# Performance work log

Hardware: AMD Instinct MI355X
Metric: run time of the kernel (lower is better)

## Reference

```python
import jax, jax.numpy as jnp
import numpy as np

BATCH, SEQ_LEN, D_MODEL, STATE_N, N_CLASSES = 32, 4096, 256, 64, 5


def setup_inputs() -> dict:
    key = jax.random.key(0)
    ks = jax.random.split(key, 9)
    x = jax.random.normal(ks[0], (BATCH, SEQ_LEN), jnp.float32)
    w_in = jax.random.normal(ks[1], (D_MODEL,), jnp.float32)
    b_in = jax.random.normal(ks[2], (D_MODEL,), jnp.float32) * 0.1
    # stable diagonal transition in (0.9, 0.999)
    A_diag = 0.9 + 0.099 * jax.random.uniform(ks[3], (D_MODEL, STATE_N), jnp.float32)
    B_in = jax.random.normal(ks[4], (D_MODEL, STATE_N), jnp.float32) * 0.1
    C_out = jax.random.normal(ks[5], (D_MODEL, STATE_N), jnp.float32) * 0.1
    D_skip = jax.random.normal(ks[6], (D_MODEL,), jnp.float32)
    W_head = jax.random.normal(ks[7], (2 * D_MODEL, N_CLASSES), jnp.float32) * 0.05
    b_head = jnp.zeros((N_CLASSES,), jnp.float32)
    return {"x": x, "w_in": w_in, "b_in": b_in, "A_diag": A_diag, "B_in": B_in,
            "C_out": C_out, "D_skip": D_skip, "W_head": W_head, "b_head": b_head}


def reference(x, w_in, b_in, A_diag, B_in, C_out, D_skip, W_head, b_head):
    # x: [B, T] scalar ECG signal; diagonal SSM recurrence over T via lax.scan
    Bsz = x.shape[0]
    D, N = A_diag.shape

    def step(s, xt):
        # xt: [B] scalar input at time t; project to channels
        u = xt[:, None] * w_in + b_in              # [B, D]
        s = A_diag * s + B_in * u[:, :, None]      # [B, D, N]
        h = jax.nn.gelu(jnp.einsum('bdn,dn->bd', s, C_out) + D_skip * u)  # [B, D]
        return s, h

    s0 = jnp.zeros((Bsz, D, N), x.dtype)
    _, h_all = jax.lax.scan(step, s0, x.T)         # h_all: [T, B, D]
    avg_p = h_all.mean(axis=0)                     # [B, D]
    max_p = h_all.max(axis=0)                      # [B, D]
    pooled = jnp.concatenate([avg_p, max_p], axis=-1)  # [B, 2D] (streaming_pool='avgmax')
    return pooled @ W_head + b_head                # [B, n_classes]
```

## Files before the change

### kernel.cpp

```cpp
#include <hip/hip_runtime.h>

#define BATCH 32
#define SEQ 4096
#define DMODEL 256
#define NCLS 5

typedef short          s8v __attribute__((ext_vector_type(8)));
typedef unsigned short u8v __attribute__((ext_vector_type(8)));
typedef float          f4v __attribute__((ext_vector_type(4)));

__device__ __forceinline__ unsigned short f2b(float f) {
    unsigned u = __float_as_uint(f);
    u += 0x7FFFu + ((u >> 16) & 1u);
    return (unsigned short)(u >> 16);
}
__device__ __forceinline__ float b2f(unsigned short u) {
    return __uint_as_float(((unsigned)u) << 16);
}

__global__ __launch_bounds__(512) void ssm_mfma_kernel(
    const float* __restrict__ x,
    const float* __restrict__ w_in,
    const float* __restrict__ b_in,
    const float* __restrict__ A_diag,
    const float* __restrict__ B_in,
    const float* __restrict__ C_out,
    const float* __restrict__ D_skip,
    float* __restrict__ pooled)
{
    __shared__ unsigned short MAb [64 * 72];
    __shared__ unsigned short CATb[64 * 72];
    __shared__ unsigned short TGb [64 * 72];
    __shared__ unsigned short Xb  [128 * 72];
    __shared__ unsigned short Sigb[128 * 72];
    __shared__ float XAf[128 * 65];
    __shared__ float Pf[64], Qf[64], Gf[64], Hf[64], Hcp[64];
    __shared__ float ps[8 * 32], pm[8 * 32];

    const int tid  = threadIdx.x;
    const int lane = tid & 63;
    const int wid  = tid >> 6;
    const int m16  = lane & 15;
    const int q4   = (lane >> 4) * 4;
    const int q8   = (lane >> 4) * 8;
    const int cb   = wid * 16;
    const int d    = blockIdx.x;

    const int   n  = lane;
    const float An = A_diag[d * 64 + n];
    const float CB = B_in[d * 64 + n] * C_out[d * 64 + n];
    const float wd = w_in[d], bd = b_in[d];
    const float Pn = CB * wd;
    const float Qn = CB * bd;
    const float Dw = D_skip[d] * wd;
    const float Db = D_skip[d] * bd;

    if (tid < 64) {
        Pf[n] = Pn; Qf[n] = Qn;
        float p = 1.0f;
        for (int m = 0; m <= 64; ++m) { XAf[m * 64 + n] = p; p *= An; }
    }
    __syncthreads();
    const float A64 = XAf[64 * 64 + n];
    const float cQ  = Qn * (1.0f - A64) / (1.0f - An);

    {
        const int r0 = tid >> 3, c0 = (tid & 7) * 8;
        #pragma unroll
        for (int jj = 0; jj < 8; ++jj) {
            const int j = c0 + jj;
            MAb [r0 * 72 + j] = f2b(XAf[(63 - j) * 64 + r0]);
            CATb[r0 * 72 + j] = f2b(XAf[(r0 + 1) * 64 + j]);
        }
        if (tid < 64) {
            float g = 0.0f, h = 0.0f;
            for (int nn = 0; nn < 64; ++nn) {
                const float pw = XAf[tid * 64 + nn];
                g = fmaf(pw, Pf[nn], g);
                h = fmaf(pw, Qf[nn], h);
            }
            Gf[tid] = g; Hf[tid] = h;
        }
    }
    __syncthreads();
    {
        const int k0 = tid >> 3, c0 = (tid & 7) * 8;
        #pragma unroll
        for (int jj = 0; jj < 8; ++jj) {
            const int j = c0 + jj;
            TGb[k0 * 72 + j] = (j <= k0) ? f2b(Gf[k0 - j]) : (unsigned short)0;
        }
        if (tid < 64) {
            float a = Db;
            for (int m = 0; m <= tid; ++m) a += Hf[m];
            Hcp[tid] = a;
        }
    }
    __syncthreads();

    s8v aMA[4][2], aCAT[4][2], aTG[4][2];
    #pragma unroll
    for (int rt = 0; rt < 4; ++rt)
        #pragma unroll
        for (int kb = 0; kb < 2; ++kb) {
            const int off = (rt * 16 + m16) * 72 + kb * 32 + q8;
            aMA [rt][kb] = *(const s8v*)&MAb [off];
            aCAT[rt][kb] = *(const s8v*)&CATb[off];
            aTG [rt][kb] = *(const s8v*)&TGb [off];
        }

    const int colA = tid >> 2;
    const int j0A  = (tid & 3) * 16;
    const float* xrow = x + (colA & 31) * SEQ + (colA >> 5) * 64 + j0A;
    unsigned short* xdst = &Xb[colA * 72 + j0A];

    float sig[4] = {0.0f, 0.0f, 0.0f, 0.0f};
    float psum = 0.0f, pmax = -1e30f;

    for (int g = 0; g < 16; ++g) {
        const float4* xg = (const float4*)(xrow + g * 256);
        const float4 u0 = xg[0], u1 = xg[1], u2 = xg[2], u3 = xg[3];
        u8v lo, hi;
        lo[0]=f2b(u0.x); lo[1]=f2b(u0.y); lo[2]=f2b(u0.z); lo[3]=f2b(u0.w);
        lo[4]=f2b(u1.x); lo[5]=f2b(u1.y); lo[6]=f2b(u1.z); lo[7]=f2b(u1.w);
        hi[0]=f2b(u2.x); hi[1]=f2b(u2.y); hi[2]=f2b(u2.z); hi[3]=f2b(u2.w);
        hi[4]=f2b(u3.x); hi[5]=f2b(u3.y); hi[6]=f2b(u3.z); hi[7]=f2b(u3.w);
        *(u8v*)(xdst)     = lo;
        *(u8v*)(xdst + 8) = hi;
        __syncthreads();

        const s8v bx0 = *(const s8v*)&Xb[(cb + m16) * 72 + q8];
        const s8v bx1 = *(const s8v*)&Xb[(cb + m16) * 72 + 32 + q8];
        #pragma unroll
        for (int rt = 0; rt < 4; ++rt) {
            f4v acc = {0.0f, 0.0f, 0.0f, 0.0f};
            acc = __builtin_amdgcn_mfma_f32_16x16x32_bf16(aMA[rt][0], bx0, acc, 0, 0, 0);
            acc = __builtin_amdgcn_mfma_f32_16x16x32_bf16(aMA[rt][1], bx1, acc, 0, 0, 0);
            #pragma unroll
            for (int r = 0; r < 4; ++r)
                XAf[(cb + m16) * 65 + rt * 16 + q4 + r] = acc[r];
        }
        __syncthreads();

        #pragma unroll
        for (int c = 0; c < 4; ++c) {
            #pragma unroll
            for (int i = 0; i < 4; ++i) {
                const int col = c * 32 + wid * 4 + i;
                Sigb[col * 72 + n] = f2b(sig[i]);
                sig[i] = fmaf(A64, sig[i], fmaf(Pn, XAf[col * 65 + n], cQ));
            }
        }
        __syncthreads();

        const s8v bs0 = *(const s8v*)&Sigb[(cb + m16) * 72 + q8];
        const s8v bs1 = *(const s8v*)&Sigb[(cb + m16) * 72 + 32 + q8];
        #pragma unroll
        for (int rt = 0; rt < 4; ++rt) {
            f4v acc = {0.0f, 0.0f, 0.0f, 0.0f};
            acc = __builtin_amdgcn_mfma_f32_16x16x32_bf16(aCAT[rt][0], bs0, acc, 0, 0, 0);
            acc = __builtin_amdgcn_mfma_f32_16x16x32_bf16(aCAT[rt][1], bs1, acc, 0, 0, 0);
            acc = __builtin_amdgcn_mfma_f32_16x16x32_bf16(aTG [rt][0], bx0, acc, 0, 0, 0);
            acc = __builtin_amdgcn_mfma_f32_16x16x32_bf16(aTG [rt][1], bx1, acc, 0, 0, 0);
            #pragma unroll
            for (int r = 0; r < 4; ++r) {
                const int k  = rt * 16 + q4 + r;
                const float xv = b2f(Xb[(cb + m16) * 72 + k]);
                const float yt = acc[r] + Hcp[k] + Dw * xv;
                const float y2 = yt * yt;
                const float zn = yt * fmaf(-0.07135481627f, y2, -1.5957691216f);
                const float h  = yt * __builtin_amdgcn_rcpf(1.0f + __expf(zn));
                psum += h;
                pmax = fmaxf(pmax, h);
            }
        }
        __syncthreads();
    }

    psum += __shfl_xor(psum, 16, 64); psum += __shfl_xor(psum, 32, 64);
    pmax = fmaxf(pmax, __shfl_xor(pmax, 16, 64));
    pmax = fmaxf(pmax, __shfl_xor(pmax, 32, 64));
    if (lane < 16) {
        ps[wid * 32 + (wid & 1) * 16 + lane] = psum;
        pm[wid * 32 + (wid & 1) * 16 + lane] = pmax;
    } else if (lane < 32) {
        const int ob = (((wid & 1) ^ 1) * 16) + (lane & 15);
        ps[wid * 32 + ob] = 0.0f;
        pm[wid * 32 + ob] = -1e30f;
    }
    __syncthreads();
    if (tid < 32) {
        float s = 0.0f, m = -1e30f;
        #pragma unroll
        for (int w = 0; w < 8; ++w) {
            s += ps[w * 32 + tid];
            m = fmaxf(m, pm[w * 32 + tid]);
        }
        pooled[tid * (2 * DMODEL) + d]          = s * (1.0f / SEQ);
        pooled[tid * (2 * DMODEL) + DMODEL + d] = m;
    }
}

__global__ __launch_bounds__(64) void head_kernel(
    const float* __restrict__ pooled,
    const float* __restrict__ W_head,
    const float* __restrict__ b_head,
    float* __restrict__ out)
{
    const int b = blockIdx.x, l = threadIdx.x;
    const float* p = pooled + b * (2 * DMODEL);
    float acc[NCLS] = {0, 0, 0, 0, 0};
    for (int k = l; k < 2 * DMODEL; k += 64) {
        const float pv = p[k];
        #pragma unroll
        for (int c = 0; c < NCLS; ++c)
            acc[c] = fmaf(pv, W_head[k * NCLS + c], acc[c]);
    }
    #pragma unroll
    for (int off = 32; off; off >>= 1)
        #pragma unroll
        for (int c = 0; c < NCLS; ++c) acc[c] += __shfl_xor(acc[c], off, 64);
    if (l == 0)
        #pragma unroll
        for (int c = 0; c < NCLS; ++c) out[b * NCLS + c] = acc[c] + b_head[c];
}

extern "C" void kernel_launch(void* const* d_in, const int* in_sizes, int n_in,
                              void* d_out, int out_size, void* d_ws, size_t ws_size,
                              hipStream_t stream) {
    const float* x      = (const float*)d_in[0];
    const float* w_in   = (const float*)d_in[1];
    const float* b_in   = (const float*)d_in[2];
    const float* A_diag = (const float*)d_in[3];
    const float* B_in   = (const float*)d_in[4];
    const float* C_out  = (const float*)d_in[5];
    const float* D_skip = (const float*)d_in[6];
    const float* W_head = (const float*)d_in[7];
    const float* b_head = (const float*)d_in[8];
    float* pooled = (float*)d_ws;
    float* out    = (float*)d_out;

    ssm_mfma_kernel<<<DMODEL, 512, 0, stream>>>(x, w_in, b_in, A_diag, B_in,
                                                C_out, D_skip, pooled);
    head_kernel<<<BATCH, 64, 0, stream>>>(pooled, W_head, b_head, out);
}
```

Measured before the change: 118.0 us.

## Remap batch columns per wave and replace chunk-state scan with in-register DPP scan

Each wave now owns four batch sequences laid out so the cross-chunk state recurrence can be done in registers with DPP row shifts and a ds_swizzle, instead of writing MFMA results to a float LDS buffer and scanning them serially with block-wide barriers. All __syncthreads in the time loop are removed, the next x chunk is prefetched from global while the current one is processed, and the bias terms (cQ, Hcp, the Dw skip) are folded into the MFMA accumulator initialisers and the Toeplitz matrix. Setup reductions are parallelised with shuffles, and the final pooling reduces within each wave. The intra-wave cross-lane data flow is intricate and depends on exact lane mappings, so a mistake would give wrong results rather than a slowdown.

```diff
diff --git a/kernel.cpp b/kernel.cpp
--- a/kernel.cpp
+++ b/kernel.cpp
@@ -5,17 +5,27 @@
 #define DMODEL 256
 #define NCLS 5
 
-typedef short          s8v __attribute__((ext_vector_type(8)));
-typedef unsigned short u8v __attribute__((ext_vector_type(8)));
-typedef float          f4v __attribute__((ext_vector_type(4)));
+typedef short          s8v  __attribute__((ext_vector_type(8)));
+typedef unsigned short u8v  __attribute__((ext_vector_type(8)));
+typedef unsigned short u4v  __attribute__((ext_vector_type(4)));
+typedef float          f4v  __attribute__((ext_vector_type(4)));
 
 __device__ __forceinline__ unsigned short f2b(float f) {
     unsigned u = __float_as_uint(f);
     u += 0x7FFFu + ((u >> 16) & 1u);
     return (unsigned short)(u >> 16);
 }
-__device__ __forceinline__ float b2f(unsigned short u) {
-    return __uint_as_float(((unsigned)u) << 16);
+__device__ __forceinline__ float dpp_shr4(float v) {
+    return __int_as_float(__builtin_amdgcn_update_dpp(
+        0, __float_as_int(v), 0x114, 0xF, 0xF, true));
+}
+__device__ __forceinline__ float dpp_shr8(float v) {
+    return __int_as_float(__builtin_amdgcn_update_dpp(
+        0, __float_as_int(v), 0x118, 0xF, 0xF, true));
+}
+__device__ __forceinline__ float swz_or12(float v) {
+    return __int_as_float(__builtin_amdgcn_ds_swizzle(
+        __float_as_int(v), 0x019F));
 }
 
 __global__ __launch_bounds__(512) void ssm_mfma_kernel(
@@ -28,72 +38,80 @@
     const float* __restrict__ D_skip,
     float* __restrict__ pooled)
 {
+    __shared__ float          Pow [65 * 64];
     __shared__ unsigned short MAb [64 * 72];
     __shared__ unsigned short CATb[64 * 72];
     __shared__ unsigned short TGb [64 * 72];
     __shared__ unsigned short Xb  [128 * 72];
     __shared__ unsigned short Sigb[128 * 72];
-    __shared__ float XAf[128 * 65];
-    __shared__ float Pf[64], Qf[64], Gf[64], Hf[64], Hcp[64];
-    __shared__ float ps[8 * 32], pm[8 * 32];
+    __shared__ float Pf[64], Qf[64], Gf[64], Hf[64], HcpS[64], Anf[64];
 
     const int tid  = threadIdx.x;
     const int lane = tid & 63;
     const int wid  = tid >> 6;
     const int m16  = lane & 15;
-    const int q4   = (lane >> 4) * 4;
-    const int q8   = (lane >> 4) * 8;
-    const int cb   = wid * 16;
+    const int q    = lane >> 4;
+    const int q4   = q * 4;
+    const int q8   = q * 8;
     const int d    = blockIdx.x;
 
-    const int   n  = lane;
-    const float An = A_diag[d * 64 + n];
-    const float CB = B_in[d * 64 + n] * C_out[d * 64 + n];
     const float wd = w_in[d], bd = b_in[d];
-    const float Pn = CB * wd;
-    const float Qn = CB * bd;
     const float Dw = D_skip[d] * wd;
     const float Db = D_skip[d] * bd;
 
+    const int bcol = wid * 4 + (m16 & 3);
+    const int cch  = m16 >> 2;
+    const int pcol = wid * 16 + m16;
+    const float* xrow = x + bcol * SEQ + cch * 64 + q * 16;
+    unsigned short* xdst = &Xb[pcol * 72 + q * 16];
+
+    float4 xl0 = ((const float4*)xrow)[0];
+    float4 xl1 = ((const float4*)xrow)[1];
+    float4 xl2 = ((const float4*)xrow)[2];
+    float4 xl3 = ((const float4*)xrow)[3];
+
     if (tid < 64) {
-        Pf[n] = Pn; Qf[n] = Qn;
+        const int n = tid;
+        const float An = A_diag[d * 64 + n];
+        const float CB = B_in[d * 64 + n] * C_out[d * 64 + n];
+        Anf[n] = An; Pf[n] = CB * wd; Qf[n] = CB * bd;
         float p = 1.0f;
-        for (int m = 0; m <= 64; ++m) { XAf[m * 64 + n] = p; p *= An; }
+        for (int m = 0; m <= 64; ++m) { Pow[m * 64 + n] = p; p *= An; }
     }
     __syncthreads();
-    const float A64 = XAf[64 * 64 + n];
-    const float cQ  = Qn * (1.0f - A64) / (1.0f - An);
-
+    {
+        const int mrow = tid >> 3, p8 = (tid & 7) * 8;
+        float g = 0.0f, h = 0.0f;
+        #pragma unroll
+        for (int jj = 0; jj < 8; ++jj) {
+            const float pw = Pow[mrow * 64 + p8 + jj];
+            g = fmaf(pw, Pf[p8 + jj], g);
+            h = fmaf(pw, Qf[p8 + jj], h);
+        }
+        g += __shfl_xor(g, 1, 64); g += __shfl_xor(g, 2, 64); g += __shfl_xor(g, 4, 64);
+        h += __shfl_xor(h, 1, 64); h += __shfl_xor(h, 2, 64); h += __shfl_xor(h, 4, 64);
+        if ((tid & 7) == 0) { Gf[mrow] = g; Hf[mrow] = h; }
+    }
+    __syncthreads();
     {
         const int r0 = tid >> 3, c0 = (tid & 7) * 8;
         #pragma unroll
         for (int jj = 0; jj < 8; ++jj) {
             const int j = c0 + jj;
-            MAb [r0 * 72 + j] = f2b(XAf[(63 - j) * 64 + r0]);
-            CATb[r0 * 72 + j] = f2b(XAf[(r0 + 1) * 64 + j]);
+            MAb [r0 * 72 + j] = f2b(Pf[r0] * Pow[(63 - j) * 64 + r0]);
+            CATb[r0 * 72 + j] = f2b(Pow[(r0 + 1) * 64 + j]);
+            TGb [r0 * 72 + j] = (j < r0)  ? f2b(Gf[r0 - j])
+                              : (j == r0) ? f2b(Gf[0] + Dw)
+                                          : (unsigned short)0;
         }
         if (tid < 64) {
-            float g = 0.0f, h = 0.0f;
-            for (int nn = 0; nn < 64; ++nn) {
-                const float pw = XAf[tid * 64 + nn];
-                g = fmaf(pw, Pf[nn], g);
-                h = fmaf(pw, Qf[nn], h);
+            float v = Hf[tid];
+            #pragma unroll
+            for (int dl = 1; dl < 64; dl <<= 1) {
+                const float t = __shfl(v, (tid - dl) & 63, 64);
+                v += (tid >= dl) ? t : 0.0f;
             }
-            Gf[tid] = g; Hf[tid] = h;
-        }
-    }
-    __syncthreads();
-    {
-        const int k0 = tid >> 3, c0 = (tid & 7) * 8;
-        #pragma unroll
-        for (int jj = 0; jj < 8; ++jj) {
-            const int j = c0 + jj;
-            TGb[k0 * 72 + j] = (j <= k0) ? f2b(Gf[k0 - j]) : (unsigned short)0;
-        }
-        if (tid < 64) {
-            float a = Db;
-            for (int m = 0; m <= tid; ++m) a += Hf[m];
-            Hcp[tid] = a;
+            HcpS[tid] = v + Db;
         }
     }
     __syncthreads();
@@ -108,65 +126,90 @@
             aCAT[rt][kb] = *(const s8v*)&CATb[off];
             aTG [rt][kb] = *(const s8v*)&TGb [off];
         }
-
-    const int colA = tid >> 2;
-    const int j0A  = (tid & 3) * 16;
-    const float* xrow = x + (colA & 31) * SEQ + (colA >> 5) * 64 + j0A;
-    unsigned short* xdst = &Xb[colA * 72 + j0A];
-
-    float sig[4] = {0.0f, 0.0f, 0.0f, 0.0f};
+    f4v cq[4], hcp[4];
+    float a64v[4][4], sig0[4][4];
+    #pragma unroll
+    for (int rt = 0; rt < 4; ++rt)
+        #pragma unroll
+        for (int r = 0; r < 4; ++r) {
+            const int nn = rt * 16 + q4 + r;
+            const float A64 = Pow[64 * 64 + nn];
+            a64v[rt][r] = A64;
+            cq[rt][r]   = Qf[nn] * (1.0f - A64) / (1.0f - Anf[nn]);
+            hcp[rt][r]  = HcpS[nn];
+            sig0[rt][r] = 0.0f;
+        }
+    const bool cc1 = (cch & 1) != 0;
+    const bool cc2 = (cch & 2) != 0;
+
+    {
+        u8v lo, hi;
+        lo[0]=f2b(xl0.x); lo[1]=f2b(xl0.y); lo[2]=f2b(xl0.z); lo[3]=f2b(xl0.w);
+        lo[4]=f2b(xl1.x); lo[5]=f2b(xl1.y); lo[6]=f2b(xl1.z); lo[7]=f2b(xl1.w);
+        hi[0]=f2b(xl2.x); hi[1]=f2b(xl2.y); hi[2]=f2b(xl2.z); hi[3]=f2b(xl2.w);
+        hi[4]=f2b(xl3.x); hi[5]=f2b(xl3.y); hi[6]=f2b(xl3.z); hi[7]=f2b(xl3.w);
+        *(u8v*)xdst       = lo;
+        *(u8v*)(xdst + 8) = hi;
+    }
+
     float psum = 0.0f, pmax = -1e30f;
 
+    #pragma unroll 1
     for (int g = 0; g < 16; ++g) {
-        const float4* xg = (const float4*)(xrow + g * 256);
-        const float4 u0 = xg[0], u1 = xg[1], u2 = xg[2], u3 = xg[3];
-        u8v lo, hi;
-        lo[0]=f2b(u0.x); lo[1]=f2b(u0.y); lo[2]=f2b(u0.z); lo[3]=f2b(u0.w);
-        lo[4]=f2b(u1.x); lo[5]=f2b(u1.y); lo[6]=f2b(u1.z); lo[7]=f2b(u1.w);
-        hi[0]=f2b(u2.x); hi[1]=f2b(u2.y); hi[2]=f2b(u2.z); hi[3]=f2b(u2.w);
-        hi[4]=f2b(u3.x); hi[5]=f2b(u3.y); hi[6]=f2b(u3.z); hi[7]=f2b(u3.w);
-        *(u8v*)(xdst)     = lo;
-        *(u8v*)(xdst + 8) = hi;
-        __syncthreads();
-
-        const s8v bx0 = *(const s8v*)&Xb[(cb + m16) * 72 + q8];
-        const s8v bx1 = *(const s8v*)&Xb[(cb + m16) * 72 + 32 + q8];
+        float4 yl0, yl1, yl2, yl3;
+        if (g < 15) {
+            const float4* xg = (const float4*)(xrow + (g + 1) * 256);
+            yl0 = xg[0]; yl1 = xg[1]; yl2 = xg[2]; yl3 = xg[3];
+        }
+        const s8v bx0 = *(const s8v*)&Xb[pcol * 72 + q8];
+        const s8v bx1 = *(const s8v*)&Xb[pcol * 72 + 32 + q8];
+        f4v vB[4];
         #pragma unroll
         for (int rt = 0; rt < 4; ++rt) {
-            f4v acc = {0.0f, 0.0f, 0.0f, 0.0f};
-            acc = __builtin_amdgcn_mfma_f32_16x16x32_bf16(aMA[rt][0], bx0, acc, 0, 0, 0);
-            acc = __builtin_amdgcn_mfma_f32_16x16x32_bf16(aMA[rt][1], bx1, acc, 0, 0, 0);
+            vB[rt] = __builtin_amdgcn_mfma_f32_16x16x32_bf16(aMA[rt][0], bx0, cq[rt], 0, 0, 0);
+            vB[rt] = __builtin_amdgcn_mfma_f32_16x16x32_bf16(aMA[rt][1], bx1, vB[rt], 0, 0, 0);
+        }
+        if (g < 15) {
+            u8v lo, hi;
+            lo[0]=f2b(yl0.x); lo[1]=f2b(yl0.y); lo[2]=f2b(yl0.z); lo[3]=f2b(yl0.w);
+            lo[4]=f2b(yl1.x); lo[5]=f2b(yl1.y); lo[6]=f2b(yl1.z); lo[7]=f2b(yl1.w);
+            hi[0]=f2b(yl2.x); hi[1]=f2b(yl2.y); hi[2]=f2b(yl2.z); hi[3]=f2b(yl2.w);
+            hi[4]=f2b(yl3.x); hi[5]=f2b(yl3.y); hi[6]=f2b(yl3.z); hi[7]=f2b(yl3.w);
+            *(u8v*)xdst       = lo;
+            *(u8v*)(xdst + 8) = hi;
+        }
+        #pragma unroll
+        for (int rt = 0; rt < 4; ++rt) {
+            u4v sg;
             #pragma unroll
-            for (int r = 0; r < 4; ++r)
-                XAf[(cb + m16) * 65 + rt * 16 + q4 + r] = acc[r];
-        }
-        __syncthreads();
-
-        #pragma unroll
-        for (int c = 0; c < 4; ++c) {
-            #pragma unroll
-            for (int i = 0; i < 4; ++i) {
-                const int col = c * 32 + wid * 4 + i;
-                Sigb[col * 72 + n] = f2b(sig[i]);
-                sig[i] = fmaf(A64, sig[i], fmaf(Pn, XAf[col * 65 + n], cQ));
+            for (int r = 0; r < 4; ++r) {
+                const float a  = a64v[rt][r];
+                const float a2 = a * a;
+                const float v  = vB[rt][r];
+                const float t1 = dpp_shr4(v);
+                const float i1 = fmaf(a, t1, v);
+                const float t2 = dpp_shr8(i1);
+                const float e  = fmaf(a, t2, t1);
+                const float ac = (cc1 ? a : 1.0f) * (cc2 ? a2 : 1.0f);
+                const float se = fmaf(ac, sig0[rt][r], e);
+                const float i2 = fmaf(a, e, v);
+                const float S  = swz_or12(i2);
+                sig0[rt][r] = fmaf(a2 * a2, sig0[rt][r], S);
+                sg[r] = f2b(se);
             }
-        }
-        __syncthreads();
-
-        const s8v bs0 = *(const s8v*)&Sigb[(cb + m16) * 72 + q8];
-        const s8v bs1 = *(const s8v*)&Sigb[(cb + m16) * 72 + 32 + q8];
+            *(u4v*)&Sigb[pcol * 72 + rt * 16 + q4] = sg;
+        }
+        const s8v bs0 = *(const s8v*)&Sigb[pcol * 72 + q8];
+        const s8v bs1 = *(const s8v*)&Sigb[pcol * 72 + 32 + q8];
         #pragma unroll
         for (int rt = 0; rt < 4; ++rt) {
-            f4v acc = {0.0f, 0.0f, 0.0f, 0.0f};
-            acc = __builtin_amdgcn_mfma_f32_16x16x32_bf16(aCAT[rt][0], bs0, acc, 0, 0, 0);
+            f4v acc = __builtin_amdgcn_mfma_f32_16x16x32_bf16(aCAT[rt][0], bs0, hcp[rt], 0, 0, 0);
             acc = __builtin_amdgcn_mfma_f32_16x16x32_bf16(aCAT[rt][1], bs1, acc, 0, 0, 0);
             acc = __builtin_amdgcn_mfma_f32_16x16x32_bf16(aTG [rt][0], bx0, acc, 0, 0, 0);
             acc = __builtin_amdgcn_mfma_f32_16x16x32_bf16(aTG [rt][1], bx1, acc, 0, 0, 0);
             #pragma unroll
             for (int r = 0; r < 4; ++r) {
-                const int k  = rt * 16 + q4 + r;
-                const float xv = b2f(Xb[(cb + m16) * 72 + k]);
-                const float yt = acc[r] + Hcp[k] + Dw * xv;
+                const float yt = acc[r];
                 const float y2 = yt * yt;
                 const float zn = yt * fmaf(-0.07135481627f, y2, -1.5957691216f);
                 const float h  = yt * __builtin_amdgcn_rcpf(1.0f + __expf(zn));
@@ -174,30 +217,17 @@
                 pmax = fmaxf(pmax, h);
             }
         }
-        __syncthreads();
-    }
-
-    psum += __shfl_xor(psum, 16, 64); psum += __shfl_xor(psum, 32, 64);
-    pmax = fmaxf(pmax, __shfl_xor(pmax, 16, 64));
-    pmax = fmaxf(pmax, __shfl_xor(pmax, 32, 64));
-    if (lane < 16) {
-        ps[wid * 32 + (wid & 1) * 16 + lane] = psum;
-        pm[wid * 32 + (wid & 1) * 16 + lane] = pmax;
-    } else if (lane < 32) {
-        const int ob = (((wid & 1) ^ 1) * 16) + (lane & 15);
-        ps[wid * 32 + ob] = 0.0f;
-        pm[wid * 32 + ob] = -1e30f;
-    }
-    __syncthreads();
-    if (tid < 32) {
-        float s = 0.0f, m = -1e30f;
-        #pragma unroll
-        for (int w = 0; w < 8; ++w) {
-            s += ps[w * 32 + tid];
-            m = fmaxf(m, pm[w * 32 + tid]);
-        }
-        pooled[tid * (2 * DMODEL) + d]          = s * (1.0f / SEQ);
-        pooled[tid * (2 * DMODEL) + DMODEL + d] = m;
+    }
+
+    #pragma unroll
+    for (int dl = 4; dl <= 32; dl <<= 1) {
+        psum += __shfl_xor(psum, dl, 64);
+        pmax  = fmaxf(pmax, __shfl_xor(pmax, dl, 64));
+    }
+    if (lane < 4) {
+        const int b = wid * 4 + lane;
+        pooled[b * (2 * DMODEL) + d]          = psum * (1.0f / SEQ);
+        pooled[b * (2 * DMODEL) + DMODEL + d] = pmax;
     }
 }
 
```

Result: faster. 108.9 us (-7.7%).
